# Kernel tuning notes

Hardware: AMD Instinct MI355X
Metric: run time of the kernel (lower is better)

The kernel has to match this reference:

```python
import jax, jax.numpy as jnp
import numpy as np

N_NODES = 100000
N_EDGES = 1600000
HID = 128


def setup_inputs() -> dict:
    key = jax.random.key(0)
    k1, k2, k3, k4, k5 = jax.random.split(key, 5)
    node_embeddings = jax.random.normal(k1, (N_NODES, HID), dtype=jnp.float32)
    src_idx = jax.random.randint(k2, (N_EDGES,), 0, N_NODES, dtype=jnp.int64)
    tgt_idx = jax.random.randint(k3, (N_EDGES,), 0, N_NODES, dtype=jnp.int64)
    # Params of the selected edge-type predictor (Linear(2h,h) -> ReLU -> Linear(h,1))
    W1 = jax.random.normal(k4, (2 * HID, HID), dtype=jnp.float32) * (1.0 / np.sqrt(2 * HID))
    b1 = jnp.zeros((HID,), dtype=jnp.float32)
    W2 = jax.random.normal(k5, (HID, 1), dtype=jnp.float32) * (1.0 / np.sqrt(HID))
    b2 = jnp.zeros((1,), dtype=jnp.float32)
    return {
        "node_embeddings": node_embeddings,
        "src_idx": src_idx,
        "tgt_idx": tgt_idx,
        "edge_type_idx": 0,
        "W1": W1,
        "b1": b1,
        "W2": W2,
        "b2": b2,
    }


def reference(node_embeddings, src_idx, tgt_idx, edge_type_idx, W1, b1, W2, b2):
    # edge_type_idx selects a predictor; params passed in are that predictor's.
    src_emb = node_embeddings[src_idx]  # [E, H]
    tgt_emb = node_embeddings[tgt_idx]  # [E, H]
    # cat([src,tgt]) @ W1 == src @ W1[:H] + tgt @ W1[H:]  (avoids materializing pair_feat)
    h = jax.nn.relu(src_emb @ W1[:HID] + tgt_emb @ W1[HID:] + b1)  # [E, H]
    out = h @ W2 + b2  # [E, 1]
    return out[:, 0]  # squeeze(-1) -> [E]
```

## Files before the change

kernel.cpp:

```cpp
#include <hip/hip_runtime.h>
#include <hip/hip_bf16.h>

#define HID 128

typedef __attribute__((ext_vector_type(8))) short short8;
typedef __attribute__((ext_vector_type(4))) float f32x4;
typedef __attribute__((ext_vector_type(16))) float f32x16;
typedef __attribute__((ext_vector_type(4))) unsigned int u32x4;
typedef __attribute__((ext_vector_type(2))) _Float16 h2;

__device__ __forceinline__ short f2bf(float x) {
    __bf16 b = (__bf16)x;
    return __builtin_bit_cast(short, b);
}
__device__ __forceinline__ float bf2f(short s) {
    unsigned u = (unsigned)(unsigned short)s << 16;
    return __builtin_bit_cast(float, u);
}


__global__ void pack_w1_uv_kernel(const float* __restrict__ W1, short* __restrict__ bpk2) {
    int t = blockIdx.x * 256 + threadIdx.x;
    int l    = t & 63;
    int ks   = (t >> 6) & 7;
    int nt   = (t >> 9) & 3;
    int half = t >> 11;
    int k0  = half * 128 + ks * 16 + (l >> 5) * 8;
    int col = nt * 32 + (l & 31);
    short8 v;
#pragma unroll
    for (int j = 0; j < 8; ++j)
        v[j] = f2bf(W1[(k0 + j) * HID + col]);
    *reinterpret_cast<short8*>(&bpk2[t * 8]) = v;
}

__global__ __launch_bounds__(512, 4) void uv_kernel(
    const float* __restrict__ emb,
    const short* __restrict__ bpk2,
    unsigned short* __restrict__ U,
    unsigned short* __restrict__ V,
    int Nn)
{
    __shared__ short lds_b[32768];

    const int tid = threadIdx.x;
    const int l   = tid & 63;
    const int wid = tid >> 6;
    const int wg  = wid >> 1;
    const int wn  = wid & 1;
    const int lc  = l & 31;
    const int hi  = l >> 5;

    {
        const u32x4* g = (const u32x4*)bpk2;
        u32x4* d = (u32x4*)lds_b;
#pragma unroll
        for (int i = 0; i < 8; ++i) d[i * 512 + tid] = g[i * 512 + tid];
    }
    __syncthreads();

    const int base = blockIdx.x * 128 + wg * 32;
    int nr = base + lc;
    if (nr >= Nn) nr = Nn - 1;

    f32x16 accU[2], accV[2];
#pragma unroll
    for (int n = 0; n < 2; ++n) { accU[n] = (f32x16)(0.f); accV[n] = (f32x16)(0.f); }

#pragma unroll
    for (int ks = 0; ks < 8; ++ks) {
        const float* p = emb + (size_t)nr * HID + ks * 16 + hi * 8;
        f32x4 x0 = *reinterpret_cast<const f32x4*>(p);
        f32x4 x1 = *reinterpret_cast<const f32x4*>(p + 4);
        short8 afr;
#pragma unroll
        for (int j = 0; j < 4; ++j) { afr[j] = f2bf(x0[j]); afr[4 + j] = f2bf(x1[j]); }
#pragma unroll
        for (int n = 0; n < 2; ++n) {
            const int nt = wn * 2 + n;
            short8 bU = *reinterpret_cast<const short8*>(&lds_b[(((0 + nt) * 8 + ks) * 64 + l) * 8]);
            short8 bV = *reinterpret_cast<const short8*>(&lds_b[(((4 + nt) * 8 + ks) * 64 + l) * 8]);
            accU[n] = __builtin_amdgcn_mfma_f32_32x32x16_bf16(afr, bU, accU[n], 0, 0, 0);
            accV[n] = __builtin_amdgcn_mfma_f32_32x32x16_bf16(afr, bV, accV[n], 0, 0, 0);
        }
    }

#pragma unroll
    for (int n = 0; n < 2; ++n) {
        const int col = wn * 64 + n * 32 + lc;
#pragma unroll
        for (int r = 0; r < 16; ++r) {
            const int row = (r & 3) + 8 * (r >> 2) + 4 * hi;
            const int node = base + row;
            if (node < Nn) {
                _Float16 hu = (_Float16)accU[n][r];
                _Float16 hv = (_Float16)accV[n][r];
                U[(size_t)node * HID + col] = __builtin_bit_cast(unsigned short, hu);
                V[(size_t)node * HID + col] = __builtin_bit_cast(unsigned short, hv);
            }
        }
    }
}

__global__ __launch_bounds__(256) void edge_pass_kernel(
    const unsigned short* __restrict__ U,
    const unsigned short* __restrict__ V,
    const void* __restrict__ src_raw,
    const void* __restrict__ tgt_raw,
    const float* __restrict__ b1,
    const float* __restrict__ W2,
    const float* __restrict__ b2,
    float* __restrict__ out,
    int E)
{
    const int tid = threadIdx.x;
    const int l   = tid & 63;
    const int wid = tid >> 6;
    const int le  = l >> 4;
    const int lc  = l & 15;

    int oddw = 0;
    {
        const int* s32 = (const int*)src_raw;
        if (l < 32) oddw = s32[2 * l + 1];
    }
    const bool i64f = (__ballot(oddw != 0) == 0ULL);

    h2 b1p[4], w2p[4];
    {
        f32x4 a = *reinterpret_cast<const f32x4*>(b1 + lc * 8);
        f32x4 b = *reinterpret_cast<const f32x4*>(b1 + lc * 8 + 4);
        f32x4 c = *reinterpret_cast<const f32x4*>(W2 + lc * 8);
        f32x4 d = *reinterpret_cast<const f32x4*>(W2 + lc * 8 + 4);
#pragma unroll
        for (int j = 0; j < 2; ++j) {
            b1p[0][j] = (_Float16)a[j];     b1p[1][j] = (_Float16)a[2 + j];
            b1p[2][j] = (_Float16)b[j];     b1p[3][j] = (_Float16)b[2 + j];
            w2p[0][j] = (_Float16)c[j];     w2p[1][j] = (_Float16)c[2 + j];
            w2p[2][j] = (_Float16)d[j];     w2p[3][j] = (_Float16)d[2 + j];
        }
    }
    const float b2s = b2[0];
    const h2 zero2 = (h2)((_Float16)0.f);

    const long long ebase = ((long long)blockIdx.x * 4 + wid) * 16;

    short8 ub[4], vb[4];
#pragma unroll
    for (int g = 0; g < 4; ++g) {
        long long e = ebase + g * 4 + le;
        if (e >= E) e = E - 1;
        long long si, ti;
        if (i64f) {
            si = ((const long long*)src_raw)[e];
            ti = ((const long long*)tgt_raw)[e];
        } else {
            si = ((const int*)src_raw)[e];
            ti = ((const int*)tgt_raw)[e];
        }
        ub[g] = *reinterpret_cast<const short8*>(U + (unsigned)si * HID + lc * 8);
        vb[g] = *reinterpret_cast<const short8*>(V + (unsigned)ti * HID + lc * 8);
    }

#pragma unroll
    for (int g = 0; g < 4; ++g) {
        const unsigned int* uw = (const unsigned int*)&ub[g];
        const unsigned int* vw = (const unsigned int*)&vb[g];
        h2 s2 = zero2;
#pragma unroll
        for (int j = 0; j < 4; ++j) {
            h2 hu = __builtin_bit_cast(h2, uw[j]);
            h2 hv = __builtin_bit_cast(h2, vw[j]);
            h2 h  = hu + hv + b1p[j];
            h = __builtin_elementwise_max(h, zero2);
            s2 = s2 + h * w2p[j];
        }
        float s = (float)s2[0] + (float)s2[1];
#pragma unroll
        for (int w = 1; w < 16; w <<= 1)
            s += __shfl_xor(s, w, 16);
        const long long e = ebase + g * 4 + le;
        if (lc == 0 && e < E)
            out[e] = s + b2s;
    }
}


__global__ void pack_w1_kernel(const float* __restrict__ W1, short* __restrict__ bpk) {
    int t = blockIdx.x * 256 + threadIdx.x;
    int f = (t >> 6) & 7;
    int l = t & 63;
    int n = t >> 9;
    int c = l & 15, kb = l >> 4;
    int k0 = f * 32 + kb * 8;
    short8 v;
#pragma unroll
    for (int j = 0; j < 8; ++j)
        v[j] = f2bf(W1[(k0 + j) * HID + n * 16 + c]);
    *reinterpret_cast<short8*>(&bpk[t * 8]) = v;
}

__global__ __launch_bounds__(256) void conv_emb_kernel(
    const float* __restrict__ emb, short* __restrict__ bemb, int n8) {
    int i = blockIdx.x * 256 + threadIdx.x;
    if (i >= n8) return;
    f32x4 x0 = *reinterpret_cast<const f32x4*>(emb + (size_t)i * 8);
    f32x4 x1 = *reinterpret_cast<const f32x4*>(emb + (size_t)i * 8 + 4);
    short8 v;
#pragma unroll
    for (int j = 0; j < 4; ++j) {
        v[j]     = f2bf(x0[j]);
        v[4 + j] = f2bf(x1[j]);
    }
    *reinterpret_cast<short8*>(&bemb[(size_t)i * 8]) = v;
}

template <int MODE>
__global__ __launch_bounds__(512, 4) void edge_head_kernel(
    const float* __restrict__ emb,
    const short* __restrict__ bemb,
    const void* __restrict__ src_raw,
    const void* __restrict__ tgt_raw,
    const float* __restrict__ W1,
    const float* __restrict__ b1,
    const float* __restrict__ W2,
    const float* __restrict__ b2,
    const short* __restrict__ bpk,
    float* __restrict__ out,
    int E)
{
    __shared__ short lds_b[32768];

    const int tid = threadIdx.x;

    int i64f = 1;
    {
        const int* s32 = (const int*)src_raw;
#pragma unroll
        for (int i = 1; i < 32; i += 2) i64f &= (s32[i] == 0);
    }

    if (MODE != 2) {
        const u32x4* g = (const u32x4*)bpk;
        u32x4* d = (u32x4*)lds_b;
#pragma unroll
        for (int i = 0; i < 8; ++i) d[i * 512 + tid] = g[i * 512 + tid];
    } else {
        for (int i = 0; i < 64; ++i) {
            int idx = i * 512 + tid;
            int col = idx & 127;
            int k   = idx >> 7;
            int n = col >> 4, cc = col & 15;
            int f = k >> 5, kb = (k >> 3) & 3, j = k & 7;
            int l2 = kb * 16 + cc;
            lds_b[(((n * 8 + f) * 64 + l2) << 3) + j] = f2bf(W1[idx]);
        }
    }
    __syncthreads();

    const int l = tid & 63;
    const int wid = tid >> 6;
    const int c = l & 15;
    const int g = l >> 4;
    const long long e0 = (long long)blockIdx.x * 256 + wid * 32;

    unsigned so[2], to[2];
#pragma unroll
    for (int m = 0; m < 2; ++m) {
        long long e = e0 + m * 16 + c;
        if (e >= E) e = E - 1;
        long long si, ti;
        if (i64f) {
            si = ((const long long*)src_raw)[e];
            ti = ((const long long*)tgt_raw)[e];
        } else {
            si = ((const int*)src_raw)[e];
            ti = ((const int*)tgt_raw)[e];
        }
        so[m] = (unsigned)si * HID;
        to[m] = (unsigned)ti * HID;
    }

    f32x4 acc[2][8];
#pragma unroll
    for (int m = 0; m < 2; ++m)
#pragma unroll
        for (int n = 0; n < 8; ++n)
            acc[m][n] = (f32x4){0.f, 0.f, 0.f, 0.f};

    const int koff = g * 8;
#pragma unroll
    for (int f = 0; f < 8; ++f) {
        short8 afr[2];
        const int k0 = (f & 3) * 32 + koff;
#pragma unroll
        for (int m = 0; m < 2; ++m) {
            const unsigned off = (f < 4 ? so[m] : to[m]) + k0;
            if (MODE == 0) {
                afr[m] = *reinterpret_cast<const short8*>(bemb + off);
            } else {
                f32x4 x0 = *reinterpret_cast<const f32x4*>(emb + off);
                f32x4 x1 = *reinterpret_cast<const f32x4*>(emb + off + 4);
                short8 t;
#pragma unroll
                for (int j = 0; j < 4; ++j) {
                    t[j]     = f2bf(x0[j]);
                    t[4 + j] = f2bf(x1[j]);
                }
                afr[m] = t;
            }
        }
#pragma unroll
        for (int n = 0; n < 8; ++n) {
            short8 bfr = *reinterpret_cast<const short8*>(&lds_b[((n * 8 + f) * 64 + l) * 8]);
#pragma unroll
            for (int m = 0; m < 2; ++m)
                acc[m][n] = __builtin_amdgcn_mfma_f32_16x16x32_bf16(afr[m], bfr, acc[m][n], 0, 0, 0);
        }
    }

    float b1v[8], w2v[8];
#pragma unroll
    for (int n = 0; n < 8; ++n) {
        b1v[n] = b1[n * 16 + c];
        w2v[n] = W2[n * 16 + c];
    }
    const float b2s = b2[0];

#pragma unroll
    for (int m = 0; m < 2; ++m) {
        float s[4] = {0.f, 0.f, 0.f, 0.f};
#pragma unroll
        for (int n = 0; n < 8; ++n) {
#pragma unroll
            for (int r = 0; r < 4; ++r)
                s[r] += fmaxf(acc[m][n][r] + b1v[n], 0.f) * w2v[n];
        }
#pragma unroll
        for (int w = 1; w < 16; w <<= 1) {
#pragma unroll
            for (int r = 0; r < 4; ++r)
                s[r] += __shfl_xor(s[r], w, 16);
        }
        if (c == 0) {
            const long long eb = e0 + m * 16 + g * 4;
#pragma unroll
            for (int r = 0; r < 4; ++r)
                if (eb + r < E) out[eb + r] = s[r] + b2s;
        }
    }
}

extern "C" void kernel_launch(void* const* d_in, const int* in_sizes, int n_in,
                              void* d_out, int out_size, void* d_ws, size_t ws_size,
                              hipStream_t stream) {
    const float* emb = (const float*)d_in[0];
    const void*  src = d_in[1];
    const void*  tgt = d_in[2];
    const float* W1 = (const float*)d_in[4];
    const float* b1 = (const float*)d_in[5];
    const float* W2 = (const float*)d_in[6];
    const float* b2 = (const float*)d_in[7];
    float* out = (float*)d_out;

    const int E  = in_sizes[1];
    const int Nn = in_sizes[0] / HID;

    const size_t uv_bytes   = (size_t)Nn * HID * sizeof(short);
    const size_t need_uv    = 65536 + 2 * uv_bytes;
    const size_t need_old   = 65536 + (size_t)in_sizes[0] * sizeof(short);

    if (ws_size >= need_uv) {
        short*          bpk2 = (short*)d_ws;
        unsigned short* U    = (unsigned short*)((char*)d_ws + 65536);
        unsigned short* Vv   = (unsigned short*)((char*)d_ws + 65536 + uv_bytes);

        pack_w1_uv_kernel<<<16, 256, 0, stream>>>(W1, bpk2);
        uv_kernel<<<(Nn + 127) / 128, 512, 0, stream>>>(emb, bpk2, U, Vv, Nn);
        edge_pass_kernel<<<(E + 63) / 64, 256, 0, stream>>>(U, Vv, src, tgt, b1, W2, b2, out, E);
        return;
    }

    short* bpk  = (short*)d_ws;
    short* bemb = (short*)((char*)d_ws + 65536);

    int mode;
    if (ws_size >= need_old)        mode = 0;
    else if (ws_size >= 65536)      mode = 1;
    else                            mode = 2;

    if (mode != 2)
        pack_w1_kernel<<<16, 256, 0, stream>>>(W1, bpk);
    if (mode == 0) {
        const int n8 = in_sizes[0] / 8;
        conv_emb_kernel<<<(n8 + 255) / 256, 256, 0, stream>>>(emb, bemb, n8);
    }

    const int grid = (E + 255) / 256;
    if (mode == 0)
        edge_head_kernel<0><<<grid, 512, 0, stream>>>(emb, bemb, src, tgt, W1, b1, W2, b2, bpk, out, E);
    else if (mode == 1)
        edge_head_kernel<1><<<grid, 512, 0, stream>>>(emb, bemb, src, tgt, W1, b1, W2, b2, bpk, out, E);
    else
        edge_head_kernel<2><<<grid, 512, 0, stream>>>(emb, bemb, src, tgt, W1, b1, W2, b2, bpk, out, E);
}
```

Baseline: 141.3 us.

## Bucket-sort edges by source node before the edge pass for gather locality

Adds a histogram, scan and scatter pipeline that counting-sorts edges into buckets of source-node ids, producing permuted src, tgt and original-index arrays. A new edge-pass kernel walks the sorted order, so U-row gathers for nearby edges hit the same cache lines, and remaps workgroups across XCDs so contiguous sorted ranges share an L2. Output is written back through the original edge index. This costs several extra kernel launches, atomic-heavy scatter passes over 1.6M edges and scattered output writes, in return for better locality on the U table.

```diff
diff --git a/kernel.cpp b/kernel.cpp
--- a/kernel.cpp
+++ b/kernel.cpp
@@ -2,20 +2,18 @@
 #include <hip/hip_bf16.h>
 
 #define HID 128
+#define NBUK 4096
 
 typedef __attribute__((ext_vector_type(8))) short short8;
 typedef __attribute__((ext_vector_type(4))) float f32x4;
 typedef __attribute__((ext_vector_type(16))) float f32x16;
 typedef __attribute__((ext_vector_type(4))) unsigned int u32x4;
+typedef __attribute__((ext_vector_type(4))) int i32x4;
 typedef __attribute__((ext_vector_type(2))) _Float16 h2;
 
 __device__ __forceinline__ short f2bf(float x) {
     __bf16 b = (__bf16)x;
     return __builtin_bit_cast(short, b);
-}
-__device__ __forceinline__ float bf2f(short s) {
-    unsigned u = (unsigned)(unsigned short)s << 16;
-    return __builtin_bit_cast(float, u);
 }
 
 
@@ -99,6 +97,168 @@
                 V[(size_t)node * HID + col] = __builtin_bit_cast(unsigned short, hv);
             }
         }
+    }
+}
+
+__global__ void zero_hist_kernel(int* __restrict__ gh) {
+    gh[blockIdx.x * 256 + threadIdx.x] = 0;
+}
+
+__global__ __launch_bounds__(256) void hist_kernel(
+    const void* __restrict__ src_raw, int E, int shift, int* __restrict__ gh)
+{
+    __shared__ int lh[NBUK];
+    const int tid = threadIdx.x;
+    for (int i = tid; i < NBUK; i += 256) lh[i] = 0;
+    __syncthreads();
+
+    int i64f = 1;
+    {
+        const int* s32 = (const int*)src_raw;
+#pragma unroll
+        for (int i = 1; i < 32; i += 2) i64f &= (s32[i] == 0);
+    }
+    const int stride = gridDim.x * 256;
+    for (int e = blockIdx.x * 256 + tid; e < E; e += stride) {
+        int s = i64f ? (int)((const long long*)src_raw)[e]
+                     : ((const int*)src_raw)[e];
+        atomicAdd(&lh[s >> shift], 1);
+    }
+    __syncthreads();
+    for (int i = tid; i < NBUK; i += 256)
+        if (lh[i]) atomicAdd(&gh[i], lh[i]);
+}
+
+__global__ __launch_bounds__(1024) void scan_kernel(
+    int* __restrict__ gh, int* __restrict__ cursor)
+{
+    __shared__ int buf[1024];
+    const int tid = threadIdx.x;
+    i32x4 v = *reinterpret_cast<const i32x4*>(&gh[tid * 4]);
+    int s = v[0] + v[1] + v[2] + v[3];
+    buf[tid] = s;
+    __syncthreads();
+#pragma unroll
+    for (int off = 1; off < 1024; off <<= 1) {
+        int x = (tid >= off) ? buf[tid - off] : 0;
+        __syncthreads();
+        buf[tid] += x;
+        __syncthreads();
+    }
+    int excl = buf[tid] - s;
+    i32x4 o;
+    o[0] = excl;
+    o[1] = o[0] + v[0];
+    o[2] = o[1] + v[1];
+    o[3] = o[2] + v[2];
+    *reinterpret_cast<i32x4*>(&cursor[tid * 4]) = o;
+}
+
+__global__ __launch_bounds__(256) void scatter_kernel(
+    const void* __restrict__ src_raw, const void* __restrict__ tgt_raw,
+    int E, int shift, int* __restrict__ cursor,
+    int* __restrict__ ss, int* __restrict__ tt, int* __restrict__ ei)
+{
+    int i64f = 1;
+    {
+        const int* s32 = (const int*)src_raw;
+#pragma unroll
+        for (int i = 1; i < 32; i += 2) i64f &= (s32[i] == 0);
+    }
+    const int stride = gridDim.x * 256;
+    for (int e = blockIdx.x * 256 + threadIdx.x; e < E; e += stride) {
+        int s, t;
+        if (i64f) {
+            s = (int)((const long long*)src_raw)[e];
+            t = (int)((const long long*)tgt_raw)[e];
+        } else {
+            s = ((const int*)src_raw)[e];
+            t = ((const int*)tgt_raw)[e];
+        }
+        int pos = atomicAdd(&cursor[s >> shift], 1);
+        ss[pos] = s;
+        tt[pos] = t;
+        ei[pos] = e;
+    }
+}
+
+__global__ __launch_bounds__(256) void edge_pass_sorted_kernel(
+    const unsigned short* __restrict__ U,
+    const unsigned short* __restrict__ V,
+    const int* __restrict__ ss,
+    const int* __restrict__ tt,
+    const int* __restrict__ ei,
+    const float* __restrict__ b1,
+    const float* __restrict__ W2,
+    const float* __restrict__ b2,
+    float* __restrict__ out,
+    int E)
+{
+    const int nwg  = gridDim.x;
+    const int orig = blockIdx.x;
+    const int q = nwg >> 3, r = nwg & 7;
+    const int xcd = orig & 7, sub = orig >> 3;
+    const int bid = (xcd < r ? xcd * (q + 1) : r * (q + 1) + (xcd - r) * q) + sub;
+
+    const int tid = threadIdx.x;
+    const int l   = tid & 63;
+    const int wid = tid >> 6;
+    const int le  = l >> 4;
+    const int lc  = l & 15;
+
+    h2 b1p[4], w2p[4];
+    {
+        f32x4 a = *reinterpret_cast<const f32x4*>(b1 + lc * 8);
+        f32x4 b = *reinterpret_cast<const f32x4*>(b1 + lc * 8 + 4);
+        f32x4 c = *reinterpret_cast<const f32x4*>(W2 + lc * 8);
+        f32x4 d = *reinterpret_cast<const f32x4*>(W2 + lc * 8 + 4);
+#pragma unroll
+        for (int j = 0; j < 2; ++j) {
+            b1p[0][j] = (_Float16)a[j];     b1p[1][j] = (_Float16)a[2 + j];
+            b1p[2][j] = (_Float16)b[j];     b1p[3][j] = (_Float16)b[2 + j];
+            w2p[0][j] = (_Float16)c[j];     w2p[1][j] = (_Float16)c[2 + j];
+            w2p[2][j] = (_Float16)d[j];     w2p[3][j] = (_Float16)d[2 + j];
+        }
+    }
+    const float b2s = b2[0];
+    const h2 zero2 = (h2)((_Float16)0.f);
+
+    const int ebase = (bid * 4 + wid) * 16;
+
+    short8 ub[4], vb[4];
+    int oid[4];
+    bool live[4];
+#pragma unroll
+    for (int g = 0; g < 4; ++g) {
+        int pos = ebase + g * 4 + le;
+        live[g] = (pos < E);
+        if (pos >= E) pos = E - 1;
+        const int s = ss[pos];
+        const int t = tt[pos];
+        oid[g] = ei[pos];
+        ub[g] = *reinterpret_cast<const short8*>(U + (unsigned)s * HID + lc * 8);
+        vb[g] = *reinterpret_cast<const short8*>(V + (unsigned)t * HID + lc * 8);
+    }
+
+#pragma unroll
+    for (int g = 0; g < 4; ++g) {
+        const unsigned int* uw = (const unsigned int*)&ub[g];
+        const unsigned int* vw = (const unsigned int*)&vb[g];
+        h2 s2 = zero2;
+#pragma unroll
+        for (int j = 0; j < 4; ++j) {
+            h2 hu = __builtin_bit_cast(h2, uw[j]);
+            h2 hv = __builtin_bit_cast(h2, vw[j]);
+            h2 h  = hu + hv + b1p[j];
+            h = __builtin_elementwise_max(h, zero2);
+            s2 = s2 + h * w2p[j];
+        }
+        float s = (float)s2[0] + (float)s2[1];
+#pragma unroll
+        for (int w = 1; w < 16; w <<= 1)
+            s += __shfl_xor(s, w, 16);
+        if (lc == 0 && live[g])
+            out[oid[g]] = s + b2s;
     }
 }
 
@@ -366,9 +526,42 @@
     const int E  = in_sizes[1];
     const int Nn = in_sizes[0] / HID;
 
-    const size_t uv_bytes   = (size_t)Nn * HID * sizeof(short);
-    const size_t need_uv    = 65536 + 2 * uv_bytes;
-    const size_t need_old   = 65536 + (size_t)in_sizes[0] * sizeof(short);
+    const size_t uv_bytes  = (size_t)Nn * HID * sizeof(short);
+    const size_t off_gh   = 65536;
+    const size_t off_cur  = off_gh + NBUK * 4;
+    const size_t off_U    = off_cur + NBUK * 4;
+    const size_t off_V    = off_U + uv_bytes;
+    const size_t off_ss   = off_V + uv_bytes;
+    const size_t off_tt   = off_ss + (size_t)E * 4;
+    const size_t off_ei   = off_tt + (size_t)E * 4;
+    const size_t need_sort = off_ei + (size_t)E * 4;
+    const size_t need_uv   = 65536 + 2 * uv_bytes;
+    const size_t need_old  = 65536 + (size_t)in_sizes[0] * sizeof(short);
+
+    if (ws_size >= need_sort) {
+        short*          bpk2   = (short*)d_ws;
+        int*            gh     = (int*)((char*)d_ws + off_gh);
+        int*            cursor = (int*)((char*)d_ws + off_cur);
+        unsigned short* U      = (unsigned short*)((char*)d_ws + off_U);
+        unsigned short* Vv     = (unsigned short*)((char*)d_ws + off_V);
+        int*            ss     = (int*)((char*)d_ws + off_ss);
+        int*            tt     = (int*)((char*)d_ws + off_tt);
+        int*            ei     = (int*)((char*)d_ws + off_ei);
+
+        int shift = 0;
+        while (((long long)(Nn - 1) >> shift) >= NBUK) ++shift;
+        if (shift < 5) shift = 5;
+
+        zero_hist_kernel<<<16, 256, 0, stream>>>(gh);
+        pack_w1_uv_kernel<<<16, 256, 0, stream>>>(W1, bpk2);
+        hist_kernel<<<256, 256, 0, stream>>>(src, E, shift, gh);
+        uv_kernel<<<(Nn + 127) / 128, 512, 0, stream>>>(emb, bpk2, U, Vv, Nn);
+        scan_kernel<<<1, 1024, 0, stream>>>(gh, cursor);
+        scatter_kernel<<<512, 256, 0, stream>>>(src, tgt, E, shift, cursor, ss, tt, ei);
+        edge_pass_sorted_kernel<<<(E + 63) / 64, 256, 0, stream>>>(
+            U, Vv, ss, tt, ei, b1, W2, b2, out, E);
+        return;
+    }
 
     if (ws_size >= need_uv) {
         short*          bpk2 = (short*)d_ws;
```

Measured after the change: 271.6 us. +92.3%, slower.
